# Optimization experiments

Measured on AMD Instinct MI355X. Metric: run time of the kernel, lower is better.

## Reference

```python
import jax, jax.numpy as jnp
import numpy as np

DIM = 1024
N_HEADS = 16
HEAD_DIM = DIM // N_HEADS
MAX_SEQ_LEN = 2048
ROPE_THETA = 10000.0


def precompute_rope_freqs(head_dim, max_seq_len, theta):
    inv_freq = 1.0 / (theta ** (jnp.arange(0, head_dim, 2, dtype=jnp.float32) / head_dim))
    t = jnp.arange(max_seq_len, dtype=jnp.float32)
    freqs = jnp.outer(t, inv_freq)                      # [T, head_dim/2]
    emb = jnp.concatenate([freqs, freqs], axis=-1)      # [T, head_dim]
    return jnp.cos(emb), jnp.sin(emb)


def rotate_half(x):
    x1, x2 = jnp.split(x, 2, axis=-1)
    return jnp.concatenate([-x2, x1], axis=-1)


def apply_rope(x, cos, sin):
    # x: [B, H, T, D], cos/sin: [T, D] -> broadcast over B, H
    return x * cos[None, None] + rotate_half(x) * sin[None, None]


def setup_inputs() -> dict:
    key = jax.random.key(0)
    kx, kq, kk, kv, ko = jax.random.split(key, 5)
    s = 1.0 / np.sqrt(DIM)
    x = jax.random.normal(kx, (2, MAX_SEQ_LEN, DIM), dtype=jnp.float32)
    wq = jax.random.normal(kq, (DIM, DIM), dtype=jnp.float32) * s
    wk = jax.random.normal(kk, (DIM, DIM), dtype=jnp.float32) * s
    wv = jax.random.normal(kv, (DIM, DIM), dtype=jnp.float32) * s
    wo = jax.random.normal(ko, (DIM, DIM), dtype=jnp.float32) * s
    cos, sin = precompute_rope_freqs(HEAD_DIM, MAX_SEQ_LEN, ROPE_THETA)
    return {"x": x, "wq": wq, "wk": wk, "wv": wv, "wo": wo, "cos": cos, "sin": sin}


def reference(x, wq, wk, wv, wo, cos, sin):
    B, T, C = x.shape
    H, D = N_HEADS, HEAD_DIM
    # nn.Linear (no bias): y = x @ W.T
    q = (x @ wq.T).reshape(B, T, H, D).transpose(0, 2, 1, 3)  # [B,H,T,D]
    k = (x @ wk.T).reshape(B, T, H, D).transpose(0, 2, 1, 3)
    v = (x @ wv.T).reshape(B, T, H, D).transpose(0, 2, 1, 3)
    q = apply_rope(q, cos[:T], sin[:T])
    k = apply_rope(k, cos[:T], sin[:T])
    scale = 1.0 / jnp.sqrt(jnp.float32(D))
    scores = jnp.einsum("bhqd,bhkd->bhqk", q, k) * scale     # [B,H,T,T]
    causal = jnp.tril(jnp.ones((T, T), dtype=bool))
    scores = jnp.where(causal[None, None], scores, -jnp.inf)
    attn = jax.nn.softmax(scores, axis=-1)
    out = jnp.einsum("bhqk,bhkd->bhqd", attn, v)             # [B,H,T,D]
    out = out.transpose(0, 2, 1, 3).reshape(B, T, C)
    return out @ wo.T
```

## Files before the change

### kernel.cpp

```cpp
#include <hip/hip_runtime.h>

typedef __attribute__((ext_vector_type(8))) short short8;
typedef __attribute__((ext_vector_type(4))) float f32x4;

#define BB 2
#define TT 2048
#define HH 16
#define DD 64
#define CC 1024

__device__ __forceinline__ unsigned short f2bf(float f) {
  union { float f; unsigned int u; } v; v.f = f;
  unsigned int r = v.u + 0x7fffu + ((v.u >> 16) & 1u);
  return (unsigned short)(r >> 16);
}
__device__ __forceinline__ float bf2f(unsigned short h) {
  union { unsigned int u; float f; } v; v.u = ((unsigned int)h) << 16; return v.f;
}

__global__ void cvt_f32_bf16(const float* __restrict__ in, unsigned short* __restrict__ out, int n) {
  int i = blockIdx.x * blockDim.x + threadIdx.x;
  int stride = gridDim.x * blockDim.x;
  for (; i < n; i += stride) out[i] = f2bf(in[i]);
}

template<bool BF16OUT>
__global__ __launch_bounds__(256) void gemm_bt(const unsigned short* __restrict__ A,
                                               const unsigned short* __restrict__ B,
                                               void* __restrict__ Cv,
                                               int M, int N, int K) {
  __shared__ unsigned short As[128 * 64];
  __shared__ unsigned short Bs[128 * 64];
  const int bm = blockIdx.y * 128, bn = blockIdx.x * 128;
  const int tid = threadIdx.x, wave = tid >> 6, lane = tid & 63;
  const int wm = (wave >> 1) * 64, wn = (wave & 1) * 64;
  const int g = lane >> 4, lr = lane & 15;
  f32x4 acc[4][4];
  #pragma unroll
  for (int i = 0; i < 4; ++i)
    #pragma unroll
    for (int j = 0; j < 4; ++j) acc[i][j] = (f32x4){0.f, 0.f, 0.f, 0.f};

  const int srow = lane >> 3, scol = (lane & 7) * 8;

  for (int k0 = 0; k0 < K; k0 += 64) {
    __syncthreads();
    #pragma unroll
    for (int c = 0; c < 4; ++c) {
      const int chunk = wave * 4 + c;
      const int row = chunk * 8 + srow;
      __builtin_amdgcn_global_load_lds(
        (const __attribute__((address_space(1))) void*)&A[(size_t)(bm + row) * K + k0 + scol],
        (__attribute__((address_space(3))) void*)&As[chunk * 512], 16, 0, 0);
      __builtin_amdgcn_global_load_lds(
        (const __attribute__((address_space(1))) void*)&B[(size_t)(bn + row) * K + k0 + scol],
        (__attribute__((address_space(3))) void*)&Bs[chunk * 512], 16, 0, 0);
    }
    __syncthreads();
    #pragma unroll
    for (int kk = 0; kk < 64; kk += 32) {
      const int kb = kk + g * 8;
      short8 af[4], bf[4];
      #pragma unroll
      for (int i = 0; i < 4; ++i) {
        af[i] = *(const short8*)&As[(wm + i * 16 + lr) * 64 + kb];
        bf[i] = *(const short8*)&Bs[(wn + i * 16 + lr) * 64 + kb];
      }
      __builtin_amdgcn_s_setprio(1);
      #pragma unroll
      for (int i = 0; i < 4; ++i)
        #pragma unroll
        for (int j = 0; j < 4; ++j)
          acc[i][j] = __builtin_amdgcn_mfma_f32_16x16x32_bf16(af[i], bf[j], acc[i][j], 0, 0, 0);
      __builtin_amdgcn_s_setprio(0);
    }
  }
  #pragma unroll
  for (int i = 0; i < 4; ++i) {
    const int row0 = bm + wm + i * 16 + g * 4;
    #pragma unroll
    for (int j = 0; j < 4; ++j) {
      const int col = bn + wn + j * 16 + lr;
      #pragma unroll
      for (int r = 0; r < 4; ++r) {
        float v = acc[i][j][r];
        if (BF16OUT) ((unsigned short*)Cv)[(size_t)(row0 + r) * N + col] = f2bf(v);
        else         ((float*)Cv)[(size_t)(row0 + r) * N + col] = v;
      }
    }
  }
}

__global__ void rope_qk(const unsigned short* __restrict__ qkv,
                        const float* __restrict__ cosb, const float* __restrict__ sinb,
                        unsigned short* __restrict__ qo, unsigned short* __restrict__ ko) {
  int idx = blockIdx.x * blockDim.x + threadIdx.x;
  int d = idx & 31;
  int h = (idx >> 5) & 15;
  int t = (idx >> 9) & 2047;
  int b = idx >> 20;
  const unsigned short* row = qkv + (size_t)(b * TT + t) * (3 * CC);
  float c = cosb[t * DD + d], s = sinb[t * DD + d];
  float q1 = bf2f(row[h * DD + d]),      q2 = bf2f(row[h * DD + d + 32]);
  float k1 = bf2f(row[CC + h * DD + d]), k2 = bf2f(row[CC + h * DD + d + 32]);
  size_t o = (((size_t)(b * HH + h)) * TT + t) * DD + d;
  const float QS = 0.125f * 1.44269504089f;
  qo[o]      = f2bf(QS * (q1 * c - q2 * s));
  qo[o + 32] = f2bf(QS * (q2 * c + q1 * s));
  ko[o]      = f2bf(k1 * c - k2 * s);
  ko[o + 32] = f2bf(k2 * c + k1 * s);
}

__global__ __launch_bounds__(256) void vtrans(const unsigned short* __restrict__ qkv,
                                              unsigned short* __restrict__ vt) {
  __shared__ unsigned short tile[64 * 72];
  const int bh = blockIdx.y, b = bh >> 4, h = bh & 15;
  const int t0 = blockIdx.x * 64;
  const int tid = threadIdx.x;
  const int r = tid >> 2, c0 = (tid & 3) * 16;
  const unsigned short* src = qkv + (size_t)(b * TT + t0 + r) * (3 * CC) + 2 * CC + h * DD + c0;
  *(short8*)&tile[r * 72 + c0]     = *(const short8*)src;
  *(short8*)&tile[r * 72 + c0 + 8] = *(const short8*)(src + 8);
  __syncthreads();
  short8 o0, o1;
  #pragma unroll
  for (int e = 0; e < 8; ++e) {
    ((unsigned short*)&o0)[e] = tile[(c0 + e) * 72 + r];
    ((unsigned short*)&o1)[e] = tile[(c0 + 8 + e) * 72 + r];
  }
  size_t dst = ((size_t)(bh * DD + r)) * TT + t0 + c0;
  *(short8*)&vt[dst]     = o0;
  *(short8*)&vt[dst + 8] = o1;
}

__global__ __launch_bounds__(256, 3) void attn5(const unsigned short* __restrict__ qb,
                                                const unsigned short* __restrict__ kb,
                                                const unsigned short* __restrict__ vt,
                                                unsigned short* __restrict__ aout) {
  __shared__ unsigned short Kbuf[2][64 * 64];
  __shared__ unsigned short Vbuf[2][64 * 64];
  __shared__ unsigned short Pw[4][16 * 72];
  const int L = blockIdx.x;
  const int xcd = L & 7, m = L >> 3;
  const int bh = xcd * 4 + (m & 3);
  const int qi = 31 - (m >> 2);
  const int qbase = qi * 64;
  const int tid = threadIdx.x, wave = tid >> 6, lane = tid & 63;
  const int g = lane >> 4, lr = lane & 15;
  const unsigned short* Qb  = qb + (size_t)bh * TT * DD;
  const unsigned short* Kb  = kb + (size_t)bh * TT * DD;
  const unsigned short* Vtb = vt + (size_t)bh * DD * TT;
  const int rowbase = qbase + wave * 16;

  short8 qf[2];
  #pragma unroll
  for (int kk = 0; kk < 2; ++kk)
    qf[kk] = *(const short8*)&Qb[(size_t)(rowbase + lr) * DD + kk * 32 + g * 8];

  f32x4 acc[4];
  float m_i[4], l_i[4];
  #pragma unroll
  for (int j = 0; j < 4; ++j) acc[j] = (f32x4){0.f, 0.f, 0.f, 0.f};
  #pragma unroll
  for (int r = 0; r < 4; ++r) { m_i[r] = -1e30f; l_i[r] = 0.f; }

  const int srow8 = lane >> 3;
  const int ssw_base = (lane & 7) * 8;

#define STAGE_KV(BUF, TI)                                                                   \
  {                                                                                         \
    const int tt = (TI);                                                                    \
    _Pragma("unroll")                                                                       \
    for (int c = 0; c < 2; ++c) {                                                           \
      const int chunk = wave * 2 + c;                                                       \
      const int row = chunk * 8 + srow8;                                                    \
      const int sw = ssw_base ^ ((row & 7) << 3);                                           \
      __builtin_amdgcn_global_load_lds(                                                     \
        (const __attribute__((address_space(1))) void*)&Kb[(size_t)(tt * 64 + row) * DD + sw], \
        (__attribute__((address_space(3))) void*)&Kbuf[BUF][chunk * 512], 16, 0, 0);        \
      __builtin_amdgcn_global_load_lds(                                                     \
        (const __attribute__((address_space(1))) void*)&Vtb[(size_t)row * TT + tt * 64 + sw], \
        (__attribute__((address_space(3))) void*)&Vbuf[BUF][chunk * 512], 16, 0, 0);        \
    }                                                                                       \
  }

  STAGE_KV(0, 0);
  __syncthreads();

  for (int t = 0; t <= qi; ++t) {
    const int cur = t & 1;
    if (t < qi) STAGE_KV(cur ^ 1, t + 1);

    f32x4 sv[4];
    #pragma unroll
    for (int j = 0; j < 4; ++j) sv[j] = (f32x4){0.f, 0.f, 0.f, 0.f};
    #pragma unroll
    for (int kk = 0; kk < 2; ++kk) {
      const int swc = (kk * 32 + g * 8) ^ ((lr & 7) << 3);
      short8 kf[4];
      #pragma unroll
      for (int j = 0; j < 4; ++j)
        kf[j] = *(const short8*)&Kbuf[cur][(j * 16 + lr) * 64 + swc];
      __builtin_amdgcn_s_setprio(1);
      #pragma unroll
      for (int j = 0; j < 4; ++j)
        sv[j] = __builtin_amdgcn_mfma_f32_16x16x32_bf16(qf[kk], kf[j], sv[j], 0, 0, 0);
      __builtin_amdgcn_s_setprio(0);
    }

    if (t == qi) {
      #pragma unroll
      for (int j = 0; j < 4; ++j)
        #pragma unroll
        for (int r = 0; r < 4; ++r) {
          int kv = t * 64 + j * 16 + lr;
          int qr = rowbase + g * 4 + r;
          if (kv > qr) sv[j][r] = -1e30f;
        }
    }
    #pragma unroll
    for (int r = 0; r < 4; ++r) {
      float mx = fmaxf(fmaxf(sv[0][r], sv[1][r]), fmaxf(sv[2][r], sv[3][r]));
      #pragma unroll
      for (int off = 1; off < 16; off <<= 1) mx = fmaxf(mx, __shfl_xor(mx, off, 64));
      float mnew = fmaxf(m_i[r], mx);
      float scl = exp2f(m_i[r] - mnew);
      m_i[r] = mnew;
      float rs = 0.f;
      #pragma unroll
      for (int j = 0; j < 4; ++j) {
        float p = exp2f(sv[j][r] - mnew);
        sv[j][r] = p;
        rs += p;
      }
      #pragma unroll
      for (int off = 1; off < 16; off <<= 1) rs += __shfl_xor(rs, off, 64);
      l_i[r] = l_i[r] * scl + rs;
      #pragma unroll
      for (int j = 0; j < 4; ++j) acc[j][r] *= scl;
    }
    #pragma unroll
    for (int j = 0; j < 4; ++j)
      #pragma unroll
      for (int r = 0; r < 4; ++r)
        Pw[wave][(g * 4 + r) * 72 + j * 16 + lr] = f2bf(sv[j][r]);
    #pragma unroll
    for (int kk = 0; kk < 2; ++kk) {
      short8 pf = *(const short8*)&Pw[wave][lr * 72 + kk * 32 + g * 8];
      const int swc = (kk * 32 + g * 8) ^ ((lr & 7) << 3);
      short8 vf[4];
      #pragma unroll
      for (int j = 0; j < 4; ++j)
        vf[j] = *(const short8*)&Vbuf[cur][(j * 16 + lr) * 64 + swc];
      __builtin_amdgcn_s_setprio(1);
      #pragma unroll
      for (int j = 0; j < 4; ++j)
        acc[j] = __builtin_amdgcn_mfma_f32_16x16x32_bf16(pf, vf[j], acc[j], 0, 0, 0);
      __builtin_amdgcn_s_setprio(0);
    }
    __syncthreads();
  }
#undef STAGE_KV

  const int b = bh >> 4, h = bh & 15;
  #pragma unroll
  for (int r = 0; r < 4; ++r) {
    float inv = 1.0f / l_i[r];
    int qr = rowbase + g * 4 + r;
    size_t rowo = ((size_t)b * TT + qr) * CC + h * DD;
    #pragma unroll
    for (int j = 0; j < 4; ++j)
      aout[rowo + j * 16 + lr] = f2bf(acc[j][r] * inv);
  }
}

extern "C" void kernel_launch(void* const* d_in, const int* in_sizes, int n_in,
                              void* d_out, int out_size, void* d_ws, size_t ws_size,
                              hipStream_t stream) {
  const float* x    = (const float*)d_in[0];
  const float* wq   = (const float*)d_in[1];
  const float* wk   = (const float*)d_in[2];
  const float* wv   = (const float*)d_in[3];
  const float* wo   = (const float*)d_in[4];
  const float* cosb = (const float*)d_in[5];
  const float* sinb = (const float*)d_in[6];
  float* out = (float*)d_out;
  char* ws = (char*)d_ws;

  const size_t MB = 1u << 20;
  unsigned short* xb    = (unsigned short*)(ws);
  unsigned short* wqkvb = (unsigned short*)(ws + 8 * MB);
  unsigned short* wob   = (unsigned short*)(ws + 14 * MB);
  unsigned short* sqkv  = (unsigned short*)(ws + 16 * MB);
  unsigned short* qb2   = (unsigned short*)(ws + 40 * MB);
  unsigned short* kb2   = (unsigned short*)(ws + 48 * MB);
  unsigned short* vtb   = (unsigned short*)(ws + 56 * MB);
  unsigned short* aoutb = (unsigned short*)(ws + 64 * MB);

  cvt_f32_bf16<<<2048, 256, 0, stream>>>(x,  xb, 4194304);
  cvt_f32_bf16<<<1024, 256, 0, stream>>>(wq, wqkvb,           1048576);
  cvt_f32_bf16<<<1024, 256, 0, stream>>>(wk, wqkvb + 1048576, 1048576);
  cvt_f32_bf16<<<1024, 256, 0, stream>>>(wv, wqkvb + 2097152, 1048576);
  cvt_f32_bf16<<<1024, 256, 0, stream>>>(wo, wob,             1048576);

  gemm_bt<true><<<dim3(24, 32), 256, 0, stream>>>(xb, wqkvb, sqkv, 4096, 3072, 1024);
  rope_qk<<<8192, 256, 0, stream>>>(sqkv, cosb, sinb, qb2, kb2);
  vtrans<<<dim3(32, 32), 256, 0, stream>>>(sqkv, vtb);
  attn5<<<1024, 256, 0, stream>>>(qb2, kb2, vtb, aoutb);
  gemm_bt<false><<<dim3(8, 32), 256, 0, stream>>>(aoutb, wob, out, 4096, 1024, 1024);
}
```

Baseline: 157.1 us.

## Transpose attention MFMA operands so each lane owns one query row

Swaps the A/B operands of both MFMAs so the score and output accumulators are laid out with one query row per lane column. The online-softmax max and sum then reduce mostly within a thread, needing only two cross-lane shuffles instead of four per row, and a single m/l state per lane. P and the output are packed to bf16 with v_cvt_pk_bf16_f32 and written as 8-byte vector stores instead of scalar 2-byte stores. This cuts shuffle, VALU and store overhead in the softmax inner loop, but the inline asm and the new layout must match the MFMA operand semantics exactly.

```diff
diff --git a/kernel.cpp b/kernel.cpp
--- a/kernel.cpp
+++ b/kernel.cpp
@@ -16,6 +16,11 @@
 }
 __device__ __forceinline__ float bf2f(unsigned short h) {
   union { unsigned int u; float f; } v; v.u = ((unsigned int)h) << 16; return v.f;
+}
+__device__ __forceinline__ unsigned int cvtpk(float lo, float hi) {
+  unsigned int r;
+  asm("v_cvt_pk_bf16_f32 %0, %1, %2" : "=v"(r) : "v"(lo), "v"(hi));
+  return r;
 }
 
 __global__ void cvt_f32_bf16(const float* __restrict__ in, unsigned short* __restrict__ out, int n) {
@@ -133,7 +138,7 @@
   *(short8*)&vt[dst + 8] = o1;
 }
 
-__global__ __launch_bounds__(256, 3) void attn5(const unsigned short* __restrict__ qb,
+__global__ __launch_bounds__(256, 3) void attn6(const unsigned short* __restrict__ qb,
                                                 const unsigned short* __restrict__ kb,
                                                 const unsigned short* __restrict__ vt,
                                                 unsigned short* __restrict__ aout) {
@@ -151,18 +156,17 @@
   const unsigned short* Kb  = kb + (size_t)bh * TT * DD;
   const unsigned short* Vtb = vt + (size_t)bh * DD * TT;
   const int rowbase = qbase + wave * 16;
+  const int myq = rowbase + lr;
 
   short8 qf[2];
   #pragma unroll
   for (int kk = 0; kk < 2; ++kk)
-    qf[kk] = *(const short8*)&Qb[(size_t)(rowbase + lr) * DD + kk * 32 + g * 8];
+    qf[kk] = *(const short8*)&Qb[(size_t)myq * DD + kk * 32 + g * 8];
 
   f32x4 acc[4];
-  float m_i[4], l_i[4];
   #pragma unroll
   for (int j = 0; j < 4; ++j) acc[j] = (f32x4){0.f, 0.f, 0.f, 0.f};
-  #pragma unroll
-  for (int r = 0; r < 4; ++r) { m_i[r] = -1e30f; l_i[r] = 0.f; }
+  float m_i = -1e30f, l_i = 0.f;
 
   const int srow8 = lane >> 3;
   const int ssw_base = (lane & 7) * 8;
@@ -204,7 +208,7 @@
       __builtin_amdgcn_s_setprio(1);
       #pragma unroll
       for (int j = 0; j < 4; ++j)
-        sv[j] = __builtin_amdgcn_mfma_f32_16x16x32_bf16(qf[kk], kf[j], sv[j], 0, 0, 0);
+        sv[j] = __builtin_amdgcn_mfma_f32_16x16x32_bf16(kf[j], qf[kk], sv[j], 0, 0, 0);
       __builtin_amdgcn_s_setprio(0);
     }
 
@@ -212,38 +216,44 @@
       #pragma unroll
       for (int j = 0; j < 4; ++j)
         #pragma unroll
-        for (int r = 0; r < 4; ++r) {
-          int kv = t * 64 + j * 16 + lr;
-          int qr = rowbase + g * 4 + r;
-          if (kv > qr) sv[j][r] = -1e30f;
-        }
-    }
-    #pragma unroll
-    for (int r = 0; r < 4; ++r) {
-      float mx = fmaxf(fmaxf(sv[0][r], sv[1][r]), fmaxf(sv[2][r], sv[3][r]));
-      #pragma unroll
-      for (int off = 1; off < 16; off <<= 1) mx = fmaxf(mx, __shfl_xor(mx, off, 64));
-      float mnew = fmaxf(m_i[r], mx);
-      float scl = exp2f(m_i[r] - mnew);
-      m_i[r] = mnew;
-      float rs = 0.f;
-      #pragma unroll
-      for (int j = 0; j < 4; ++j) {
+        for (int r = 0; r < 4; ++r)
+          if (t * 64 + j * 16 + g * 4 + r > myq) sv[j][r] = -1e30f;
+    }
+
+    float mx = -1e30f;
+    #pragma unroll
+    for (int j = 0; j < 4; ++j)
+      #pragma unroll
+      for (int r = 0; r < 4; ++r) mx = fmaxf(mx, sv[j][r]);
+    mx = fmaxf(mx, __shfl_xor(mx, 16, 64));
+    mx = fmaxf(mx, __shfl_xor(mx, 32, 64));
+    float mnew = fmaxf(m_i, mx);
+    float scl = exp2f(m_i - mnew);
+    m_i = mnew;
+    float rs = 0.f;
+    #pragma unroll
+    for (int j = 0; j < 4; ++j)
+      #pragma unroll
+      for (int r = 0; r < 4; ++r) {
         float p = exp2f(sv[j][r] - mnew);
         sv[j][r] = p;
         rs += p;
       }
-      #pragma unroll
-      for (int off = 1; off < 16; off <<= 1) rs += __shfl_xor(rs, off, 64);
-      l_i[r] = l_i[r] * scl + rs;
-      #pragma unroll
-      for (int j = 0; j < 4; ++j) acc[j][r] *= scl;
-    }
+    rs += __shfl_xor(rs, 16, 64);
+    rs += __shfl_xor(rs, 32, 64);
+    l_i = l_i * scl + rs;
     #pragma unroll
     for (int j = 0; j < 4; ++j)
       #pragma unroll
-      for (int r = 0; r < 4; ++r)
-        Pw[wave][(g * 4 + r) * 72 + j * 16 + lr] = f2bf(sv[j][r]);
+      for (int r = 0; r < 4; ++r) acc[j][r] *= scl;
+
+    #pragma unroll
+    for (int j = 0; j < 4; ++j) {
+      uint2 pk;
+      pk.x = cvtpk(sv[j][0], sv[j][1]);
+      pk.y = cvtpk(sv[j][2], sv[j][3]);
+      *(uint2*)&Pw[wave][lr * 72 + j * 16 + g * 4] = pk;
+    }
     #pragma unroll
     for (int kk = 0; kk < 2; ++kk) {
       short8 pf = *(const short8*)&Pw[wave][lr * 72 + kk * 32 + g * 8];
@@ -255,7 +265,7 @@
       __builtin_amdgcn_s_setprio(1);
       #pragma unroll
       for (int j = 0; j < 4; ++j)
-        acc[j] = __builtin_amdgcn_mfma_f32_16x16x32_bf16(pf, vf[j], acc[j], 0, 0, 0);
+        acc[j] = __builtin_amdgcn_mfma_f32_16x16x32_bf16(vf[j], pf, acc[j], 0, 0, 0);
       __builtin_amdgcn_s_setprio(0);
     }
     __syncthreads();
@@ -263,14 +273,14 @@
 #undef STAGE_KV
 
   const int b = bh >> 4, h = bh & 15;
-  #pragma unroll
-  for (int r = 0; r < 4; ++r) {
-    float inv = 1.0f / l_i[r];
-    int qr = rowbase + g * 4 + r;
-    size_t rowo = ((size_t)b * TT + qr) * CC + h * DD;
-    #pragma unroll
-    for (int j = 0; j < 4; ++j)
-      aout[rowo + j * 16 + lr] = f2bf(acc[j][r] * inv);
+  const float inv = 1.0f / l_i;
+  size_t rowo = ((size_t)b * TT + myq) * CC + h * DD;
+  #pragma unroll
+  for (int j = 0; j < 4; ++j) {
+    uint2 pk;
+    pk.x = cvtpk(acc[j][0] * inv, acc[j][1] * inv);
+    pk.y = cvtpk(acc[j][2] * inv, acc[j][3] * inv);
+    *(uint2*)&aout[rowo + j * 16 + g * 4] = pk;
   }
 }
 
@@ -306,6 +316,6 @@
   gemm_bt<true><<<dim3(24, 32), 256, 0, stream>>>(xb, wqkvb, sqkv, 4096, 3072, 1024);
   rope_qk<<<8192, 256, 0, stream>>>(sqkv, cosb, sinb, qb2, kb2);
   vtrans<<<dim3(32, 32), 256, 0, stream>>>(sqkv, vtb);
-  attn5<<<1024, 256, 0, stream>>>(qb2, kb2, vtb, aoutb);
+  attn6<<<1024, 256, 0, stream>>>(qb2, kb2, vtb, aoutb);
   gemm_bt<false><<<dim3(8, 32), 256, 0, stream>>>(aoutb, wob, out, 4096, 1024, 1024);
 }
```

After: 134.1 us. 1.17x faster.
